# Kernel tuning notes

Measured on AMD Instinct MI355X. Metric: run time of the kernel, lower is better.

Reference implementation:

```python
import jax, jax.numpy as jnp
import numpy as np

HIDDEN = 1024
HEADS = 16
HEAD_DIM = HIDDEN // HEADS


def setup_inputs() -> dict:
    key = jax.random.key(0)
    k1, k2, k3, k4 = jax.random.split(key, 4)
    x = jax.random.normal(k1, (4, 2048, HIDDEN), dtype=jnp.float32)
    # qkv: Linear(hidden, 3*hidden, bias=False) -> weight [3*hidden, hidden]
    w_qkv = jax.random.normal(k2, (3 * HIDDEN, HIDDEN), dtype=jnp.float32) * (HIDDEN ** -0.5)
    # out_proj: Linear(hidden, hidden) with bias
    w_out = jax.random.normal(k3, (HIDDEN, HIDDEN), dtype=jnp.float32) * (HIDDEN ** -0.5)
    b_out = jax.random.normal(k4, (HIDDEN,), dtype=jnp.float32) * 0.01
    return {"x": x, "w_qkv": w_qkv, "w_out": w_out, "b_out": b_out}


def reference(x, w_qkv, w_out, b_out):
    B, N, _ = x.shape
    scale = HEAD_DIM ** -0.5
    qkv = jnp.einsum('bnc,dc->bnd', x, w_qkv)            # [B,N,3*hidden]
    qkv = qkv.reshape(B, N, 3, HEADS, HEAD_DIM)
    qkv = jnp.transpose(qkv, (2, 0, 3, 1, 4))            # [3,B,H,N,hd]
    q, k, v = qkv[0], qkv[1], qkv[2]
    att = jnp.einsum('bhxd,bhyd->bhxy', q, k) * scale    # [B,H,N,N]
    att = jax.nn.softmax(att, axis=-1)
    out = jnp.einsum('bhxy,bhyd->bhxd', att, v)          # [B,H,N,hd]
    out = jnp.transpose(out, (0, 2, 1, 3)).reshape(B, N, HIDDEN)
    out = jnp.einsum('bnc,dc->bnd', out, w_out) + b_out
    return out
```

## Files before the change

### kernel.cpp

```cpp
#include <hip/hip_runtime.h>

typedef unsigned short u16;
typedef short short8 __attribute__((ext_vector_type(8)));
typedef float f32x4 __attribute__((ext_vector_type(4)));
typedef float f32x16 __attribute__((ext_vector_type(16)));
typedef unsigned short u16x4 __attribute__((ext_vector_type(4)));
typedef unsigned int u32x4 __attribute__((ext_vector_type(4)));

#define MFMA16(a, b, c) __builtin_amdgcn_mfma_f32_16x16x32_bf16((a), (b), (c), 0, 0, 0)
#define MFMA32(a, b, c) __builtin_amdgcn_mfma_f32_32x32x16_bf16((a), (b), (c), 0, 0, 0)

#if __has_builtin(__builtin_amdgcn_exp2f)
#define EXP2F(x) __builtin_amdgcn_exp2f(x)
#else
#define EXP2F(x) exp2f(x)
#endif

__device__ __forceinline__ u16 f2bf(float f) {
    unsigned u = __builtin_bit_cast(unsigned, f);
    u += 0x7FFFu + ((u >> 16) & 1u);
    return (u16)(u >> 16);
}

__device__ __forceinline__ void async16(void* lds, const void* g) {
    __builtin_amdgcn_global_load_lds(
        (const __attribute__((address_space(1))) void*)g,
        (__attribute__((address_space(3))) void*)lds, 16, 0, 0);
}

__device__ __forceinline__ unsigned cvtpk(float lo, float hi) {
    unsigned r;
    asm("v_cvt_pk_bf16_f32 %0, %1, %2" : "=v"(r) : "v"(lo), "v"(hi));
    return r;
}
__device__ __forceinline__ void plswap(unsigned& a, unsigned& b) {
    asm("v_permlane32_swap_b32 %0, %1" : "+v"(a), "+v"(b));
}

__device__ __forceinline__ void packP(const f32x16& s, short8& f0, short8& f1) {
    u32x4 u0, u1;
    {
        unsigned a = cvtpk(s[0], s[1]), b = cvtpk(s[4], s[5]);
        plswap(a, b);
        unsigned c = cvtpk(s[2], s[3]), d = cvtpk(s[6], s[7]);
        plswap(c, d);
        u0[0] = a; u0[1] = c; u0[2] = b; u0[3] = d;
    }
    {
        unsigned a = cvtpk(s[8], s[9]), b = cvtpk(s[12], s[13]);
        plswap(a, b);
        unsigned c = cvtpk(s[10], s[11]), d = cvtpk(s[14], s[15]);
        plswap(c, d);
        u1[0] = a; u1[1] = c; u1[2] = b; u1[3] = d;
    }
    f0 = __builtin_bit_cast(short8, u0);
    f1 = __builtin_bit_cast(short8, u1);
}

__global__ __launch_bounds__(256) void castk(const float* __restrict__ in,
                                             u16* __restrict__ out, int n, int scaleCut) {
    int i = (blockIdx.x * 256 + threadIdx.x) * 4;
    if (i >= n) return;
    float4 v = *(const float4*)(in + i);
    float sc = (i < scaleCut) ? 0.18033688011112042f : 1.0f;
    u16x4 r;
    r[0] = f2bf(v.x * sc); r[1] = f2bf(v.y * sc);
    r[2] = f2bf(v.z * sc); r[3] = f2bf(v.w * sc);
    *(u16x4*)(out + i) = r;
}

template <int MODE>
__global__ __launch_bounds__(256, 2) void gemm_bt(const u16* __restrict__ A,
                                                  const u16* __restrict__ B,
                                                  void* __restrict__ C0,
                                                  void* __restrict__ C1,
                                                  int M, int N, int K) {
    __shared__ u16 As[128 * 32];
    __shared__ u16 Bs[128 * 32];
    const int tid = threadIdx.x;
    const int w = tid >> 6, l = tid & 63;
    const int g = l >> 4, lo = l & 15;
    const int mtiles = M >> 7;
    const int tm = blockIdx.x % mtiles, tn = blockIdx.x / mtiles;
    const int rowBase = tm << 7, colBase = tn << 7;
    const int wrow = w >> 1, wcol = w & 1;

    f32x4 acc[4][4] = {};

    const int srow = l >> 2;
    const int scol = (l & 3) * 8;
    const int nk = K >> 5;
    for (int kt = 0; kt < nk; ++kt) {
        const int kbase = kt * 32 + scol;
#pragma unroll
        for (int it = 0; it < 2; ++it) {
            const int seg = it * 4 + w;
            const int r = seg * 16 + srow;
            async16(&As[seg * 512], &A[(size_t)(rowBase + r) * K + kbase]);
            async16(&Bs[seg * 512], &B[(size_t)(colBase + r) * K + kbase]);
        }
        __syncthreads();
        short8 af[4], bf[4];
#pragma unroll
        for (int mi = 0; mi < 4; ++mi)
            af[mi] = *(const short8*)&As[(wrow * 64 + mi * 16 + lo) * 32 + g * 8];
#pragma unroll
        for (int ni = 0; ni < 4; ++ni)
            bf[ni] = *(const short8*)&Bs[(wcol * 64 + ni * 16 + lo) * 32 + g * 8];
#pragma unroll
        for (int mi = 0; mi < 4; ++mi)
#pragma unroll
            for (int ni = 0; ni < 4; ++ni)
                acc[mi][ni] = MFMA16(af[mi], bf[ni], acc[mi][ni]);
        __syncthreads();
    }

    if constexpr (MODE == 0) {
        if (colBase < 2048) {
            u16* qk = (u16*)C0;
#pragma unroll
            for (int ni = 0; ni < 4; ++ni) {
                const int c = colBase + wcol * 64 + ni * 16 + lo;
#pragma unroll
                for (int mi = 0; mi < 4; ++mi) {
                    const int r0 = rowBase + wrow * 64 + mi * 16 + g * 4;
#pragma unroll
                    for (int i = 0; i < 4; ++i)
                        qk[(size_t)(r0 + i) * 2048 + c] = f2bf(acc[mi][ni][i]);
                }
            }
        } else {
            u16* vt = (u16*)C1;
            const int b = rowBase >> 11;
#pragma unroll
            for (int ni = 0; ni < 4; ++ni) {
                const int c = colBase + wcol * 64 + ni * 16 + lo;
                const int hh = (c - 2048) >> 6, d = (c - 2048) & 63;
                u16* vrow = vt + ((size_t)((b * 16 + hh) * 64 + d)) * 2048;
#pragma unroll
                for (int mi = 0; mi < 4; ++mi) {
                    const int r0 = rowBase + wrow * 64 + mi * 16 + g * 4;
                    u16x4 pk;
#pragma unroll
                    for (int i = 0; i < 4; ++i) pk[i] = f2bf(acc[mi][ni][i]);
                    *(u16x4*)(vrow + (r0 & 2047)) = pk;
                }
            }
        }
    } else {
        float* Cf = (float*)C0;
        const float* bias = (const float*)C1;
#pragma unroll
        for (int ni = 0; ni < 4; ++ni) {
            const int c = colBase + wcol * 64 + ni * 16 + lo;
            const float bv = bias[c];
#pragma unroll
            for (int mi = 0; mi < 4; ++mi) {
                const int r0 = rowBase + wrow * 64 + mi * 16 + g * 4;
#pragma unroll
                for (int i = 0; i < 4; ++i)
                    Cf[(size_t)(r0 + i) * N + c] = acc[mi][ni][i] + bv;
            }
        }
    }
}

__global__ __launch_bounds__(256, 3) void attn_fwd(const u16* __restrict__ qkb,
                                                   const u16* __restrict__ vtg,
                                                   u16* __restrict__ outb) {
    __shared__ u16 Ks[2][64 * 64];
    __shared__ u16 Vs[2][64 * 64];
    __shared__ float Abuf[4][32];
    const int tid = threadIdx.x;
    const int w = tid >> 6, l = tid & 63;
    const int hi = l >> 5, lq = l & 31;

    int lin = (blockIdx.x & 7) * 128 + (blockIdx.x >> 3);
    const int bh = lin >> 4, qt = lin & 15;
    const int b = bh >> 4, h = bh & 15;
    const int q0 = qt * 128 + w * 32;
    const size_t rowQ = (size_t)b * 2048 + q0;

    short8 qf[4];
#pragma unroll
    for (int ks = 0; ks < 4; ++ks)
        qf[ks] = *(const short8*)(qkb + (rowQ + lq) * 2048 + h * 64 + ks * 16 + hi * 8);

    int koff[2][4];
#pragma unroll
    for (int t = 0; t < 2; ++t)
#pragma unroll
        for (int ks = 0; ks < 4; ++ks) {
            const int row = t * 32 + lq;
            koff[t][ks] = (row * 128 + ks * 32 + hi * 16) ^ ((row & 7) << 4);
        }

    const int L0 = tid * 16, L1 = tid * 16 + 4096;
    const int kr0 = L0 >> 7, kc0 = ((L0 ^ ((kr0 & 7) << 4)) & 127) >> 1;
    const int kr1 = L1 >> 7, kc1 = ((L1 ^ ((kr1 & 7) << 4)) & 127) >> 1;
    const u16* ks0 = qkb + (size_t)(b * 2048 + kr0) * 2048 + 1024 + h * 64 + kc0;
    const u16* ks1 = qkb + (size_t)(b * 2048 + kr1) * 2048 + 1024 + h * 64 + kc1;
    const u16* vs0 = vtg + ((size_t)bh * 64 + kr0) * 2048 + kc0;
    const u16* vs1 = vtg + ((size_t)bh * 64 + kr1) * 2048 + kc1;
    const size_t KADV = (size_t)64 * 2048;

    f32x16 O0, O1;
#pragma unroll
    for (int i = 0; i < 16; ++i) { O0[i] = 0.f; O1[i] = 0.f; }
    float mrun = -1e30f, lsum = 0.f;

    async16((char*)Ks[0] + L0, ks0); async16((char*)Ks[0] + L1, ks1);
    async16((char*)Vs[0] + L0, vs0); async16((char*)Vs[0] + L1, vs1);
    ks0 += KADV; ks1 += KADV; vs0 += 64; vs1 += 64;

    int cur = 0;
    for (int kt = 0; kt < 32; ++kt) {
        __syncthreads();
        if (kt < 31) {
            const int nx = cur ^ 1;
            async16((char*)Ks[nx] + L0, ks0); async16((char*)Ks[nx] + L1, ks1);
            async16((char*)Vs[nx] + L0, vs0); async16((char*)Vs[nx] + L1, vs1);
            ks0 += KADV; ks1 += KADV; vs0 += 64; vs1 += 64;
        }
        const char* kb = (const char*)Ks[cur];
        const char* vb = (const char*)Vs[cur];

        f32x16 s0, s1;
#pragma unroll
        for (int i = 0; i < 16; ++i) { s0[i] = 0.f; s1[i] = 0.f; }
#pragma unroll
        for (int ks = 0; ks < 4; ++ks) {
            const short8 k0 = *(const short8*)(kb + koff[0][ks]);
            const short8 k1 = *(const short8*)(kb + koff[1][ks]);
            s0 = MFMA32(k0, qf[ks], s0);
            s1 = MFMA32(k1, qf[ks], s1);
        }

        float pmax = s0[0];
#pragma unroll
        for (int i = 1; i < 16; ++i) pmax = fmaxf(pmax, s0[i]);
#pragma unroll
        for (int i = 0; i < 16; ++i) pmax = fmaxf(pmax, s1[i]);
        pmax = fmaxf(pmax, __shfl_xor(pmax, 32));

        if (!__all(pmax - mrun <= 10.f)) {
            const float mn = fmaxf(mrun, pmax);
            const float al = EXP2F(mrun - mn);
            mrun = mn;
            lsum *= al;
            Abuf[w][lq] = al;
#pragma unroll
            for (int r = 0; r < 16; ++r) {
                const float a2 = Abuf[w][(r & 3) + 8 * (r >> 2) + 4 * hi];
                O0[r] *= a2; O1[r] *= a2;
            }
        }
        float sum = 0.f;
#pragma unroll
        for (int i = 0; i < 16; ++i) { const float p = EXP2F(s0[i] - mrun); s0[i] = p; sum += p; }
#pragma unroll
        for (int i = 0; i < 16; ++i) { const float p = EXP2F(s1[i] - mrun); s1[i] = p; sum += p; }
        sum += __shfl_xor(sum, 32);
        lsum += sum;

        short8 pf[2][2];
        packP(s0, pf[0][0], pf[0][1]);
        packP(s1, pf[1][0], pf[1][1]);

#pragma unroll
        for (int t = 0; t < 2; ++t)
#pragma unroll
            for (int ksl = 0; ksl < 2; ++ksl) {
                const int kstep = t * 2 + ksl;
                const short8 v0 = *(const short8*)(vb + koff[0][kstep]);
                const short8 v1 = *(const short8*)(vb + koff[1][kstep]);
                O0 = MFMA32(pf[t][ksl], v0, O0);
                O1 = MFMA32(pf[t][ksl], v1, O1);
            }
        cur ^= 1;
    }

    Abuf[w][lq] = 1.f / lsum;
#pragma unroll
    for (int r = 0; r < 16; ++r) {
        const int qrow = (r & 3) + 8 * (r >> 2) + 4 * hi;
        const float linv = Abuf[w][qrow];
        u16* op = outb + (rowQ + qrow) * 1024 + h * 64 + lq;
        op[0] = f2bf(O0[r] * linv);
        op[32] = f2bf(O1[r] * linv);
    }
}

extern "C" void kernel_launch(void* const* d_in, const int* in_sizes, int n_in,
                              void* d_out, int out_size, void* d_ws, size_t ws_size,
                              hipStream_t stream) {
    const float* x     = (const float*)d_in[0];
    const float* w_qkv = (const float*)d_in[1];
    const float* w_out = (const float*)d_in[2];
    const float* b_out = (const float*)d_in[3];
    float* out = (float*)d_out;

    u16* xb    = (u16*)d_ws;
    u16* wqkvb = xb    + (size_t)8192 * 1024;
    u16* woutb = wqkvb + (size_t)3072 * 1024;
    u16* qkb   = woutb + (size_t)1024 * 1024;
    u16* vtg   = qkb   + (size_t)8192 * 2048;
    u16* attb  = vtg   + (size_t)64 * 64 * 2048;

    castk<<<8192, 256, 0, stream>>>(x, xb, 8192 * 1024, 0);
    castk<<<3072, 256, 0, stream>>>(w_qkv, wqkvb, 3072 * 1024, 1024 * 1024);
    castk<<<1024, 256, 0, stream>>>(w_out, woutb, 1024 * 1024, 0);

    gemm_bt<0><<<dim3((8192 / 128) * (3072 / 128)), 256, 0, stream>>>(
        xb, wqkvb, qkb, vtg, 8192, 3072, 1024);

    attn_fwd<<<1024, 256, 0, stream>>>(qkb, vtg, attb);

    gemm_bt<1><<<dim3((8192 / 128) * (1024 / 128)), 256, 0, stream>>>(
        attb, woutb, out, (void*)b_out, 8192, 1024, 1024);
}
```

Measured before the change: 198.0 us.

## Compute softmax row sums via MFMA with ones, split key tile into halves

The attention kernel now processes each 64-key tile as two 32-key halves, each with its own running-max update. This halves the live score registers. The softmax denominator is accumulated with extra MFMAs against a ones vector, replacing the scalar sum reductions and shuffles, and the final normalization reads it directly from that accumulator. It also raises the launch-bounds occupancy target from 3 to 4 and adds s_setprio around the MFMA groups. The cost is extra MFMA work for the sums and more frequent rescale checks, and the sum is now taken over bf16-rounded P values.

```diff
diff --git a/kernel.cpp b/kernel.cpp
--- a/kernel.cpp
+++ b/kernel.cpp
@@ -35,6 +35,9 @@
 }
 __device__ __forceinline__ void plswap(unsigned& a, unsigned& b) {
     asm("v_permlane32_swap_b32 %0, %1" : "+v"(a), "+v"(b));
+}
+__device__ __forceinline__ float max3f(float a, float b, float c) {
+    return fmaxf(fmaxf(a, b), c);
 }
 
 __device__ __forceinline__ void packP(const f32x16& s, short8& f0, short8& f1) {
@@ -165,7 +168,7 @@
     }
 }
 
-__global__ __launch_bounds__(256, 3) void attn_fwd(const u16* __restrict__ qkb,
+__global__ __launch_bounds__(256, 4) void attn_fwd(const u16* __restrict__ qkb,
                                                    const u16* __restrict__ vtg,
                                                    u16* __restrict__ outb) {
     __shared__ u16 Ks[2][64 * 64];
@@ -175,25 +178,20 @@
     const int w = tid >> 6, l = tid & 63;
     const int hi = l >> 5, lq = l & 31;
 
-    int lin = (blockIdx.x & 7) * 128 + (blockIdx.x >> 3);
+    const int lin = (blockIdx.x & 7) * 128 + (blockIdx.x >> 3);
     const int bh = lin >> 4, qt = lin & 15;
     const int b = bh >> 4, h = bh & 15;
-    const int q0 = qt * 128 + w * 32;
-    const size_t rowQ = (size_t)b * 2048 + q0;
+    const size_t rowQ = (size_t)b * 2048 + qt * 128 + w * 32;
 
     short8 qf[4];
 #pragma unroll
     for (int ks = 0; ks < 4; ++ks)
         qf[ks] = *(const short8*)(qkb + (rowQ + lq) * 2048 + h * 64 + ks * 16 + hi * 8);
 
-    int koff[2][4];
-#pragma unroll
-    for (int t = 0; t < 2; ++t)
-#pragma unroll
-        for (int ks = 0; ks < 4; ++ks) {
-            const int row = t * 32 + lq;
-            koff[t][ks] = (row * 128 + ks * 32 + hi * 16) ^ ((row & 7) << 4);
-        }
+    int koff[4];
+#pragma unroll
+    for (int ks = 0; ks < 4; ++ks)
+        koff[ks] = (lq * 128 + ks * 32 + hi * 16) ^ ((lq & 7) << 4);
 
     const int L0 = tid * 16, L1 = tid * 16 + 4096;
     const int kr0 = L0 >> 7, kc0 = ((L0 ^ ((kr0 & 7) << 4)) & 127) >> 1;
@@ -204,10 +202,11 @@
     const u16* vs1 = vtg + ((size_t)bh * 64 + kr1) * 2048 + kc1;
     const size_t KADV = (size_t)64 * 2048;
 
-    f32x16 O0, O1;
-#pragma unroll
-    for (int i = 0; i < 16; ++i) { O0[i] = 0.f; O1[i] = 0.f; }
-    float mrun = -1e30f, lsum = 0.f;
+    f32x16 O0, O1, Ol;
+#pragma unroll
+    for (int i = 0; i < 16; ++i) { O0[i] = 0.f; O1[i] = 0.f; Ol[i] = 0.f; }
+    float mrun = -1e30f;
+    const short8 onesv = {16256, 16256, 16256, 16256, 16256, 16256, 16256, 16256};
 
     async16((char*)Ks[0] + L0, ks0); async16((char*)Ks[0] + L1, ks1);
     async16((char*)Vs[0] + L0, vs0); async16((char*)Vs[0] + L1, vs1);
@@ -225,66 +224,58 @@
         const char* kb = (const char*)Ks[cur];
         const char* vb = (const char*)Vs[cur];
 
-        f32x16 s0, s1;
-#pragma unroll
-        for (int i = 0; i < 16; ++i) { s0[i] = 0.f; s1[i] = 0.f; }
-#pragma unroll
-        for (int ks = 0; ks < 4; ++ks) {
-            const short8 k0 = *(const short8*)(kb + koff[0][ks]);
-            const short8 k1 = *(const short8*)(kb + koff[1][ks]);
-            s0 = MFMA32(k0, qf[ks], s0);
-            s1 = MFMA32(k1, qf[ks], s1);
-        }
-
-        float pmax = s0[0];
-#pragma unroll
-        for (int i = 1; i < 16; ++i) pmax = fmaxf(pmax, s0[i]);
-#pragma unroll
-        for (int i = 0; i < 16; ++i) pmax = fmaxf(pmax, s1[i]);
-        pmax = fmaxf(pmax, __shfl_xor(pmax, 32));
-
-        if (!__all(pmax - mrun <= 10.f)) {
-            const float mn = fmaxf(mrun, pmax);
-            const float al = EXP2F(mrun - mn);
-            mrun = mn;
-            lsum *= al;
-            Abuf[w][lq] = al;
-#pragma unroll
-            for (int r = 0; r < 16; ++r) {
-                const float a2 = Abuf[w][(r & 3) + 8 * (r >> 2) + 4 * hi];
-                O0[r] *= a2; O1[r] *= a2;
+#pragma unroll
+        for (int t = 0; t < 2; ++t) {
+            const int tb = t * 4096;
+            f32x16 s;
+#pragma unroll
+            for (int i = 0; i < 16; ++i) s[i] = 0.f;
+            __builtin_amdgcn_s_setprio(1);
+#pragma unroll
+            for (int ks = 0; ks < 4; ++ks)
+                s = MFMA32(*(const short8*)(kb + koff[ks] + tb), qf[ks], s);
+            __builtin_amdgcn_s_setprio(0);
+
+            float m0 = max3f(s[0], s[1], s[2]),  m1 = max3f(s[3], s[4], s[5]);
+            float m2 = max3f(s[6], s[7], s[8]),  m3 = max3f(s[9], s[10], s[11]);
+            float m4 = max3f(s[12], s[13], s[14]);
+            float pmax = max3f(max3f(m0, m1, m2), max3f(m3, m4, s[15]),
+                               fmaxf(s[15], m4));
+            pmax = fmaxf(pmax, __shfl_xor(pmax, 32));
+
+            if (!__all(pmax - mrun <= 10.f)) {
+                const float mn = fmaxf(mrun, pmax);
+                const float al = EXP2F(mrun - mn);
+                mrun = mn;
+                Abuf[w][lq] = al;
+#pragma unroll
+                for (int r = 0; r < 16; ++r) {
+                    const float a2 = Abuf[w][(r & 3) + 8 * (r >> 2) + 4 * hi];
+                    O0[r] *= a2; O1[r] *= a2; Ol[r] *= a2;
+                }
             }
-        }
-        float sum = 0.f;
-#pragma unroll
-        for (int i = 0; i < 16; ++i) { const float p = EXP2F(s0[i] - mrun); s0[i] = p; sum += p; }
-#pragma unroll
-        for (int i = 0; i < 16; ++i) { const float p = EXP2F(s1[i] - mrun); s1[i] = p; sum += p; }
-        sum += __shfl_xor(sum, 32);
-        lsum += sum;
-
-        short8 pf[2][2];
-        packP(s0, pf[0][0], pf[0][1]);
-        packP(s1, pf[1][0], pf[1][1]);
-
-#pragma unroll
-        for (int t = 0; t < 2; ++t)
-#pragma unroll
-            for (int ksl = 0; ksl < 2; ++ksl) {
-                const int kstep = t * 2 + ksl;
-                const short8 v0 = *(const short8*)(vb + koff[0][kstep]);
-                const short8 v1 = *(const short8*)(vb + koff[1][kstep]);
-                O0 = MFMA32(pf[t][ksl], v0, O0);
-                O1 = MFMA32(pf[t][ksl], v1, O1);
-            }
+#pragma unroll
+            for (int i = 0; i < 16; ++i) s[i] = EXP2F(s[i] - mrun);
+
+            short8 p0, p1;
+            packP(s, p0, p1);
+
+            __builtin_amdgcn_s_setprio(1);
+            Ol = MFMA32(p0, onesv, Ol);
+            Ol = MFMA32(p1, onesv, Ol);
+            O0 = MFMA32(p0, *(const short8*)(vb + koff[t * 2]), O0);
+            O1 = MFMA32(p0, *(const short8*)(vb + koff[t * 2] + 4096), O1);
+            O0 = MFMA32(p1, *(const short8*)(vb + koff[t * 2 + 1]), O0);
+            O1 = MFMA32(p1, *(const short8*)(vb + koff[t * 2 + 1] + 4096), O1);
+            __builtin_amdgcn_s_setprio(0);
+        }
         cur ^= 1;
     }
 
-    Abuf[w][lq] = 1.f / lsum;
 #pragma unroll
     for (int r = 0; r < 16; ++r) {
         const int qrow = (r & 3) + 8 * (r >> 2) + 4 * hi;
-        const float linv = Abuf[w][qrow];
+        const float linv = 1.0f / Ol[r];
         u16* op = outb + (rowQ + qrow) * 1024 + h * 64 + lq;
         op[0] = f2bf(O0[r] * linv);
         op[32] = f2bf(O1[r] * linv);
```

Measured after the change: 200.6 us. No clear change (+1.3%).
